# Optimization experiments

Hardware: AMD Instinct MI355X
Metric: run time of the kernel (lower is better)

## Reference

```python
import jax, jax.numpy as jnp
import numpy as np


def setup_inputs() -> dict:
    B, n, C = 256, 512, 256
    key = jax.random.key(0)
    ks = jax.random.split(key, 8)
    s = 1.0 / np.sqrt(C)
    return {
        "P": jax.random.normal(ks[0], (B, n, C), dtype=jnp.float32),
        "id": jax.random.randint(ks[1], (B,), 0, n, dtype=jnp.int64),
        "Wq": jax.random.normal(ks[2], (C, C), dtype=jnp.float32) * s,
        "bq": jax.random.normal(ks[3], (C,), dtype=jnp.float32) * s,
        "Wk": jax.random.normal(ks[4], (C, C), dtype=jnp.float32) * s,
        "bk": jax.random.normal(ks[5], (C,), dtype=jnp.float32) * s,
        "Wv": jax.random.normal(ks[6], (C, C), dtype=jnp.float32) * s,
        "bv": jax.random.normal(ks[7], (C,), dtype=jnp.float32) * s,
    }


def reference(P, id, Wq, bq, Wk, bk, Wv, bv):
    # Gather the query row per batch first, then project (same math as
    # projecting all rows and gathering, but avoids redundant compute).
    B = P.shape[0]
    p_sel = P[jnp.arange(B), id]                 # [B, C]
    Q = p_sel @ Wq.T + bq                        # [B, C]
    K = jnp.einsum('bnc,dc->bnd', P, Wk) + bk    # [B, n, C]
    V = jnp.einsum('bnc,dc->bnd', P, Wv) + bv    # [B, n, C]
    scores = jnp.einsum('bc,bnc->bn', Q, K)      # [B, n] (no sqrt scaling, per source)
    attn = jax.nn.softmax(scores, axis=-1)       # [B, n]
    out = jnp.einsum('bn,bnc->bc', attn, V)      # [B, C]
    return out
```

## Files before the change

### kernel.cpp

```cpp
#include <hip/hip_runtime.h>

#define BATCH 256
#define NROW  512
#define CDIM  256
#define SPLIT 8
#define CHUNK (NROW / SPLIT)
#define WPB   4
#define RPW   (CHUNK / WPB)
#define CHK   4
#define NCHK  (RPW / CHK)

#define DOT4(a, b) ((a).x * (b).x + (a).y * (b).y + (a).z * (b).z + (a).w * (b).w)

__global__ __launch_bounds__(256) void qk_kernel(
    const float* __restrict__ P, const int* __restrict__ idx,
    const float* __restrict__ Wq, const float* __restrict__ bq,
    const float* __restrict__ Wk, float* __restrict__ qk) {
  const int b = blockIdx.x;
  const int t = threadIdx.x;
  const int lane = t & 63;
  const int w = t >> 6;

  __shared__ float s_psel[CDIM];
  __shared__ float s_q[CDIM];
  __shared__ float s_qkp[WPB][CDIM];

  s_psel[t] = P[((size_t)b * NROW + (size_t)idx[b]) * CDIM + t];
  __syncthreads();

  const float4 pr4 = ((const float4*)s_psel)[lane];

  const int d0 = w * 64;
#pragma unroll
  for (int g = 0; g < 8; ++g) {
    float4 wq[8];
#pragma unroll
    for (int i = 0; i < 8; ++i)
      wq[i] = ((const float4*)(Wq + (size_t)(d0 + g * 8 + i) * CDIM))[lane];
#pragma unroll
    for (int i = 0; i < 8; ++i) {
      float part = DOT4(wq[i], pr4);
#pragma unroll
      for (int mm = 32; mm >= 1; mm >>= 1) part += __shfl_xor(part, mm, 64);
      if (lane == 0) s_q[d0 + g * 8 + i] = part + bq[d0 + g * 8 + i];
    }
  }
  __syncthreads();

  {
    float4 acc = make_float4(0.f, 0.f, 0.f, 0.f);
#pragma unroll 8
    for (int dd = 0; dd < 64; ++dd) {
      const int d = d0 + dd;
      const float qd = s_q[d];
      const float4 wk4 = ((const float4*)(Wk + (size_t)d * CDIM))[lane];
      acc.x += qd * wk4.x; acc.y += qd * wk4.y;
      acc.z += qd * wk4.z; acc.w += qd * wk4.w;
    }
    ((float4*)s_qkp[w])[lane] = acc;
  }
  __syncthreads();

  qk[(size_t)b * CDIM + t] =
      s_qkp[0][t] + s_qkp[1][t] + s_qkp[2][t] + s_qkp[3][t];
}

__global__ __launch_bounds__(256, 8) void attn_part_kernel(
    const float* __restrict__ P, const float* __restrict__ qk,
    float* __restrict__ ctxp, float* __restrict__ mp, float* __restrict__ lp) {
  const int bs = blockIdx.x;
  const int b = bs >> 3;
  const int s = bs & (SPLIT - 1);
  const int t = threadIdx.x;
  const int lane = t & 63;
  const int w = t >> 6;

  __shared__ float s_ctx[WPB][CDIM];
  __shared__ float s_m[WPB], s_l[WPB];

  const float* Pw =
      P + ((size_t)b * NROW + (size_t)s * CHUNK + (size_t)w * RPW) * CDIM;

  float4 pv0[CHK], pv1[CHK];
#pragma unroll
  for (int i = 0; i < CHK; ++i)
    pv0[i] = ((const float4*)(Pw + (size_t)i * CDIM))[lane];

  const float4 qk4 = ((const float4*)(qk + (size_t)b * CDIM))[lane];

  float m = -1e30f, l = 0.f;
  float4 ctx = make_float4(0.f, 0.f, 0.f, 0.f);

#define PREFETCH(dst, chn)                                                   \
  {                                                                          \
    _Pragma("unroll") for (int i = 0; i < CHK; ++i) dst[i] =                 \
        ((const float4*)(Pw + (size_t)((chn) * CHK + i) * CDIM))[lane];      \
  }

#define CONSUME(cur)                                                         \
  {                                                                          \
    float sc[CHK];                                                           \
    _Pragma("unroll") for (int i = 0; i < CHK; ++i) {                        \
      float part = DOT4(cur[i], qk4);                                        \
      _Pragma("unroll") for (int mm = 32; mm >= 1; mm >>= 1)                 \
          part += __shfl_xor(part, mm, 64);                                  \
      sc[i] = part;                                                          \
    }                                                                        \
    float cmax = sc[0];                                                      \
    _Pragma("unroll") for (int i = 1; i < CHK; ++i)                          \
        cmax = fmaxf(cmax, sc[i]);                                           \
    const float mnew = fmaxf(m, cmax);                                       \
    const float scale = __expf(m - mnew);       \
    l *= scale;                                                              \
    ctx.x *= scale; ctx.y *= scale; ctx.z *= scale; ctx.w *= scale;          \
    _Pragma("unroll") for (int i = 0; i < CHK; ++i) {                        \
      const float p = __expf(sc[i] - mnew);                                  \
      l += p;                                                                \
      ctx.x += p * cur[i].x; ctx.y += p * cur[i].y;                          \
      ctx.z += p * cur[i].z; ctx.w += p * cur[i].w;                          \
    }                                                                        \
    m = mnew;                                                                \
  }

#pragma unroll
  for (int cc = 0; cc < NCHK; cc += 2) {
    if (cc + 1 < NCHK) PREFETCH(pv1, cc + 1);
    CONSUME(pv0);
    if (cc + 2 < NCHK) PREFETCH(pv0, cc + 2);
    if (cc + 1 < NCHK) CONSUME(pv1);
  }
#undef PREFETCH
#undef CONSUME

  ((float4*)s_ctx[w])[lane] = ctx;
  if (lane == 0) { s_m[w] = m; s_l[w] = l; }
  __syncthreads();

  float mb = fmaxf(fmaxf(s_m[0], s_m[1]), fmaxf(s_m[2], s_m[3]));
  float co0 = __expf(s_m[0] - mb), co1 = __expf(s_m[1] - mb);
  float co2 = __expf(s_m[2] - mb), co3 = __expf(s_m[3] - mb);
  ctxp[(size_t)bs * CDIM + t] = co0 * s_ctx[0][t] + co1 * s_ctx[1][t] +
                                co2 * s_ctx[2][t] + co3 * s_ctx[3][t];
  if (t == 0) {
    mp[bs] = mb;
    lp[bs] = co0 * s_l[0] + co1 * s_l[1] + co2 * s_l[2] + co3 * s_l[3];
  }
}

__global__ __launch_bounds__(256) void combine_kernel(
    const float* __restrict__ ctxp, const float* __restrict__ mp,
    const float* __restrict__ lp, const float* __restrict__ Wv,
    const float* __restrict__ bv, float* __restrict__ out) {
  const int b = blockIdx.x;
  const int t = threadIdx.x;
  const int lane = t & 63;
  const int w = t >> 6;

  __shared__ float s_ctxn[CDIM];

  {
    float ms[SPLIT];
    float mg = -3.4e38f;
#pragma unroll
    for (int i = 0; i < SPLIT; ++i) {
      ms[i] = mp[b * SPLIT + i];
      mg = fmaxf(mg, ms[i]);
    }
    float ww[SPLIT];
    float lg = 0.f;
#pragma unroll
    for (int i = 0; i < SPLIT; ++i) {
      ww[i] = __expf(ms[i] - mg);
      lg += lp[b * SPLIT + i] * ww[i];
    }
    float c = 0.f;
#pragma unroll
    for (int i = 0; i < SPLIT; ++i)
      c += ctxp[(size_t)(b * SPLIT + i) * CDIM + t] * ww[i];
    s_ctxn[t] = c / lg;
  }
  __syncthreads();

  const float4 cx4 = ((const float4*)s_ctxn)[lane];
  const int d0 = w * 64;
#pragma unroll
  for (int g = 0; g < 8; ++g) {
    float4 wv[8];
#pragma unroll
    for (int i = 0; i < 8; ++i)
      wv[i] = ((const float4*)(Wv + (size_t)(d0 + g * 8 + i) * CDIM))[lane];
#pragma unroll
    for (int i = 0; i < 8; ++i) {
      float part = DOT4(wv[i], cx4);
#pragma unroll
      for (int mm = 32; mm >= 1; mm >>= 1) part += __shfl_xor(part, mm, 64);
      if (lane == 0) {
        const int d = d0 + g * 8 + i;
        out[(size_t)b * CDIM + d] = part + bv[d];
      }
    }
  }
}

extern "C" void kernel_launch(void* const* d_in, const int* in_sizes, int n_in,
                              void* d_out, int out_size, void* d_ws,
                              size_t ws_size, hipStream_t stream) {
  const float* P  = (const float*)d_in[0];
  const int*  idx = (const int*)d_in[1];
  const float* Wq = (const float*)d_in[2];
  const float* bq = (const float*)d_in[3];
  const float* Wk = (const float*)d_in[4];
  const float* Wv = (const float*)d_in[6];
  const float* bv = (const float*)d_in[7];
  float* out = (float*)d_out;

  float* ws   = (float*)d_ws;
  float* qk   = ws;
  float* ctxp = qk + BATCH * CDIM;
  float* mp   = ctxp + BATCH * SPLIT * CDIM;
  float* lp   = mp + BATCH * SPLIT;

  qk_kernel<<<BATCH, 256, 0, stream>>>(P, idx, Wq, bq, Wk, qk);
  attn_part_kernel<<<BATCH * SPLIT, 256, 0, stream>>>(P, qk, ctxp, mp, lp);
  combine_kernel<<<BATCH, 256, 0, stream>>>(ctxp, mp, lp, Wv, bv, out);
}
```

Before: 256.1 us.

## Precompute fused Wq·Wk matrix and transposed Wv, batch qk and combine

Adds a prep kernel that computes the fused matrix M = Wq^T Wk and the bias term bq·Wk, and writes a transposed copy of Wv. With these, the qk and combine kernels become simple per-thread column GEMVs that handle 4 or 8 batches per block, reusing weight loads across batches. The attention kernel now issues all 16 rows of loads up front with CHK=8 in place of the double-buffered loop, and its occupancy hint drops to 4. This adds an extra launch and a 256x256x256 matmul run by only 32 blocks on every call, which may sit on the critical path.

```diff
diff --git a/kernel.cpp b/kernel.cpp
--- a/kernel.cpp
+++ b/kernel.cpp
@@ -7,65 +7,81 @@
 #define CHUNK (NROW / SPLIT)
 #define WPB   4
 #define RPW   (CHUNK / WPB)
-#define CHK   4
-#define NCHK  (RPW / CHK)
+#define CHK   8
 
 #define DOT4(a, b) ((a).x * (b).x + (a).y * (b).y + (a).z * (b).z + (a).w * (b).w)
+
+__global__ __launch_bounds__(256) void prep_kernel(
+    const float* __restrict__ Wq, const float* __restrict__ bq,
+    const float* __restrict__ Wk, const float* __restrict__ Wv,
+    float* __restrict__ MT, float* __restrict__ c0, float* __restrict__ WvT) {
+  const int t = threadIdx.x;
+
+  if (blockIdx.x < 16) {
+    __shared__ float s_wq[CDIM][16];
+    __shared__ float s_bq[CDIM];
+    const int cbase = blockIdx.x * 16;
+#pragma unroll
+    for (int it = 0; it < 16; ++it) {
+      const int d = it * 16 + (t >> 4);
+      s_wq[d][t & 15] = Wq[(size_t)d * CDIM + cbase + (t & 15)];
+    }
+    if (blockIdx.x == 0) s_bq[t] = bq[t];
+    __syncthreads();
+
+    float acc[16];
+#pragma unroll
+    for (int j = 0; j < 16; ++j) acc[j] = 0.f;
+    float accc0 = 0.f;
+    for (int d = 0; d < CDIM; ++d) {
+      const float wkv = Wk[(size_t)d * CDIM + t];
+#pragma unroll
+      for (int j = 0; j < 16; ++j) acc[j] += s_wq[d][j] * wkv;
+      if (blockIdx.x == 0) accc0 += s_bq[d] * wkv;
+    }
+#pragma unroll
+    for (int j = 0; j < 16; ++j) MT[(size_t)(cbase + j) * CDIM + t] = acc[j];
+    if (blockIdx.x == 0) c0[t] = accc0;
+  } else {
+    __shared__ float s_wv[16][CDIM + 1];
+    const int rbase = (blockIdx.x - 16) * 16;
+#pragma unroll
+    for (int r = 0; r < 16; ++r)
+      s_wv[r][t] = Wv[(size_t)(rbase + r) * CDIM + t];
+    __syncthreads();
+#pragma unroll
+    for (int it = 0; it < 16; ++it) {
+      const int c = it * 16 + (t >> 4);
+      WvT[(size_t)c * CDIM + rbase + (t & 15)] = s_wv[t & 15][c];
+    }
+  }
+}
 
 __global__ __launch_bounds__(256) void qk_kernel(
     const float* __restrict__ P, const int* __restrict__ idx,
-    const float* __restrict__ Wq, const float* __restrict__ bq,
-    const float* __restrict__ Wk, float* __restrict__ qk) {
-  const int b = blockIdx.x;
-  const int t = threadIdx.x;
-  const int lane = t & 63;
-  const int w = t >> 6;
-
-  __shared__ float s_psel[CDIM];
-  __shared__ float s_q[CDIM];
-  __shared__ float s_qkp[WPB][CDIM];
-
-  s_psel[t] = P[((size_t)b * NROW + (size_t)idx[b]) * CDIM + t];
+    const float* __restrict__ MT, const float* __restrict__ c0,
+    float* __restrict__ qk) {
+  const int t = threadIdx.x;
+  const int b0 = blockIdx.x * 4;
+
+  __shared__ float s_ps[4][CDIM];
+#pragma unroll
+  for (int j = 0; j < 4; ++j)
+    s_ps[j][t] = P[((size_t)(b0 + j) * NROW + (size_t)idx[b0 + j]) * CDIM + t];
   __syncthreads();
 
-  const float4 pr4 = ((const float4*)s_psel)[lane];
-
-  const int d0 = w * 64;
-#pragma unroll
-  for (int g = 0; g < 8; ++g) {
-    float4 wq[8];
-#pragma unroll
-    for (int i = 0; i < 8; ++i)
-      wq[i] = ((const float4*)(Wq + (size_t)(d0 + g * 8 + i) * CDIM))[lane];
-#pragma unroll
-    for (int i = 0; i < 8; ++i) {
-      float part = DOT4(wq[i], pr4);
-#pragma unroll
-      for (int mm = 32; mm >= 1; mm >>= 1) part += __shfl_xor(part, mm, 64);
-      if (lane == 0) s_q[d0 + g * 8 + i] = part + bq[d0 + g * 8 + i];
-    }
-  }
-  __syncthreads();
-
-  {
-    float4 acc = make_float4(0.f, 0.f, 0.f, 0.f);
-#pragma unroll 8
-    for (int dd = 0; dd < 64; ++dd) {
-      const int d = d0 + dd;
-      const float qd = s_q[d];
-      const float4 wk4 = ((const float4*)(Wk + (size_t)d * CDIM))[lane];
-      acc.x += qd * wk4.x; acc.y += qd * wk4.y;
-      acc.z += qd * wk4.z; acc.w += qd * wk4.w;
-    }
-    ((float4*)s_qkp[w])[lane] = acc;
-  }
-  __syncthreads();
-
-  qk[(size_t)b * CDIM + t] =
-      s_qkp[0][t] + s_qkp[1][t] + s_qkp[2][t] + s_qkp[3][t];
-}
-
-__global__ __launch_bounds__(256, 8) void attn_part_kernel(
+  float acc[4] = {0.f, 0.f, 0.f, 0.f};
+  for (int c = 0; c < CDIM; ++c) {
+    const float mtv = MT[(size_t)c * CDIM + t];
+#pragma unroll
+    for (int j = 0; j < 4; ++j) acc[j] += s_ps[j][c] * mtv;
+  }
+  const float cc = c0[t];
+#pragma unroll
+  for (int j = 0; j < 4; ++j) qk[(size_t)(b0 + j) * CDIM + t] = acc[j] + cc;
+}
+
+__global__ __launch_bounds__(256, 4) void attn_part_kernel(
     const float* __restrict__ P, const float* __restrict__ qk,
     float* __restrict__ ctxp, float* __restrict__ mp, float* __restrict__ lp) {
   const int bs = blockIdx.x;
@@ -81,21 +97,18 @@
   const float* Pw =
       P + ((size_t)b * NROW + (size_t)s * CHUNK + (size_t)w * RPW) * CDIM;
 
+  const float4 qk4 = ((const float4*)(qk + (size_t)b * CDIM))[lane];
+
   float4 pv0[CHK], pv1[CHK];
 #pragma unroll
   for (int i = 0; i < CHK; ++i)
     pv0[i] = ((const float4*)(Pw + (size_t)i * CDIM))[lane];
-
-  const float4 qk4 = ((const float4*)(qk + (size_t)b * CDIM))[lane];
+#pragma unroll
+  for (int i = 0; i < CHK; ++i)
+    pv1[i] = ((const float4*)(Pw + (size_t)(CHK + i) * CDIM))[lane];
 
   float m = -1e30f, l = 0.f;
   float4 ctx = make_float4(0.f, 0.f, 0.f, 0.f);
-
-#define PREFETCH(dst, chn)                                                   \
-  {                                                                          \
-    _Pragma("unroll") for (int i = 0; i < CHK; ++i) dst[i] =                 \
-        ((const float4*)(Pw + (size_t)((chn) * CHK + i) * CDIM))[lane];      \
-  }
 
 #define CONSUME(cur)                                                         \
   {                                                                          \
@@ -110,7 +123,7 @@
     _Pragma("unroll") for (int i = 1; i < CHK; ++i)                          \
         cmax = fmaxf(cmax, sc[i]);                                           \
     const float mnew = fmaxf(m, cmax);                                       \
-    const float scale = __expf(m - mnew);       \
+    const float scale = __expf(m - mnew);      \
     l *= scale;                                                              \
     ctx.x *= scale; ctx.y *= scale; ctx.z *= scale; ctx.w *= scale;          \
     _Pragma("unroll") for (int i = 0; i < CHK; ++i) {                        \
@@ -122,23 +135,17 @@
     m = mnew;                                                                \
   }
 
-#pragma unroll
-  for (int cc = 0; cc < NCHK; cc += 2) {
-    if (cc + 1 < NCHK) PREFETCH(pv1, cc + 1);
-    CONSUME(pv0);
-    if (cc + 2 < NCHK) PREFETCH(pv0, cc + 2);
-    if (cc + 1 < NCHK) CONSUME(pv1);
-  }
-#undef PREFETCH
+  CONSUME(pv0);
+  CONSUME(pv1);
 #undef CONSUME
 
   ((float4*)s_ctx[w])[lane] = ctx;
   if (lane == 0) { s_m[w] = m; s_l[w] = l; }
   __syncthreads();
 
-  float mb = fmaxf(fmaxf(s_m[0], s_m[1]), fmaxf(s_m[2], s_m[3]));
-  float co0 = __expf(s_m[0] - mb), co1 = __expf(s_m[1] - mb);
-  float co2 = __expf(s_m[2] - mb), co3 = __expf(s_m[3] - mb);
+  const float mb = fmaxf(fmaxf(s_m[0], s_m[1]), fmaxf(s_m[2], s_m[3]));
+  const float co0 = __expf(s_m[0] - mb), co1 = __expf(s_m[1] - mb);
+  const float co2 = __expf(s_m[2] - mb), co3 = __expf(s_m[3] - mb);
   ctxp[(size_t)bs * CDIM + t] = co0 * s_ctx[0][t] + co1 * s_ctx[1][t] +
                                 co2 * s_ctx[2][t] + co3 * s_ctx[3][t];
   if (t == 0) {
@@ -149,16 +156,16 @@
 
 __global__ __launch_bounds__(256) void combine_kernel(
     const float* __restrict__ ctxp, const float* __restrict__ mp,
-    const float* __restrict__ lp, const float* __restrict__ Wv,
+    const float* __restrict__ lp, const float* __restrict__ WvT,
     const float* __restrict__ bv, float* __restrict__ out) {
-  const int b = blockIdx.x;
-  const int t = threadIdx.x;
-  const int lane = t & 63;
-  const int w = t >> 6;
-
-  __shared__ float s_ctxn[CDIM];
-
-  {
+  const int t = threadIdx.x;
+  const int b0 = blockIdx.x * 8;
+
+  __shared__ float s_ctxn[8][CDIM];
+
+#pragma unroll
+  for (int j = 0; j < 8; ++j) {
+    const int b = b0 + j;
     float ms[SPLIT];
     float mg = -3.4e38f;
 #pragma unroll
@@ -166,40 +173,26 @@
       ms[i] = mp[b * SPLIT + i];
       mg = fmaxf(mg, ms[i]);
     }
-    float ww[SPLIT];
-    float lg = 0.f;
+    float lg = 0.f, c = 0.f;
 #pragma unroll
     for (int i = 0; i < SPLIT; ++i) {
-      ww[i] = __expf(ms[i] - mg);
-      lg += lp[b * SPLIT + i] * ww[i];
-    }
-    float c = 0.f;
-#pragma unroll
-    for (int i = 0; i < SPLIT; ++i)
-      c += ctxp[(size_t)(b * SPLIT + i) * CDIM + t] * ww[i];
-    s_ctxn[t] = c / lg;
+      const float ww = __expf(ms[i] - mg);
+      lg += lp[b * SPLIT + i] * ww;
+      c += ctxp[(size_t)(b * SPLIT + i) * CDIM + t] * ww;
+    }
+    s_ctxn[j][t] = c / lg;
   }
   __syncthreads();
 
-  const float4 cx4 = ((const float4*)s_ctxn)[lane];
-  const int d0 = w * 64;
-#pragma unroll
-  for (int g = 0; g < 8; ++g) {
-    float4 wv[8];
-#pragma unroll
-    for (int i = 0; i < 8; ++i)
-      wv[i] = ((const float4*)(Wv + (size_t)(d0 + g * 8 + i) * CDIM))[lane];
-#pragma unroll
-    for (int i = 0; i < 8; ++i) {
-      float part = DOT4(wv[i], cx4);
-#pragma unroll
-      for (int mm = 32; mm >= 1; mm >>= 1) part += __shfl_xor(part, mm, 64);
-      if (lane == 0) {
-        const int d = d0 + g * 8 + i;
-        out[(size_t)b * CDIM + d] = part + bv[d];
-      }
-    }
-  }
+  float acc[8] = {0.f, 0.f, 0.f, 0.f, 0.f, 0.f, 0.f, 0.f};
+  for (int c = 0; c < CDIM; ++c) {
+    const float wvt = WvT[(size_t)c * CDIM + t];
+#pragma unroll
+    for (int j = 0; j < 8; ++j) acc[j] += s_ctxn[j][c] * wvt;
+  }
+  const float bvt = bv[t];
+#pragma unroll
+  for (int j = 0; j < 8; ++j) out[(size_t)(b0 + j) * CDIM + t] = acc[j] + bvt;
 }
 
 extern "C" void kernel_launch(void* const* d_in, const int* in_sizes, int n_in,
@@ -215,12 +208,16 @@
   float* out = (float*)d_out;
 
   float* ws   = (float*)d_ws;
-  float* qk   = ws;
+  float* MT   = ws;
+  float* c0   = MT + CDIM * CDIM;
+  float* WvT  = c0 + CDIM;
+  float* qk   = WvT + CDIM * CDIM;
   float* ctxp = qk + BATCH * CDIM;
   float* mp   = ctxp + BATCH * SPLIT * CDIM;
   float* lp   = mp + BATCH * SPLIT;
 
-  qk_kernel<<<BATCH, 256, 0, stream>>>(P, idx, Wq, bq, Wk, qk);
+  prep_kernel<<<32, 256, 0, stream>>>(Wq, bq, Wk, Wv, MT, c0, WvT);
+  qk_kernel<<<BATCH / 4, 256, 0, stream>>>(P, idx, MT, c0, qk);
   attn_part_kernel<<<BATCH * SPLIT, 256, 0, stream>>>(P, qk, ctxp, mp, lp);
-  combine_kernel<<<BATCH, 256, 0, stream>>>(ctxp, mp, lp, Wv, bv, out);
-}
+  combine_kernel<<<BATCH / 8, 256, 0, stream>>>(ctxp, mp, lp, WvT, bv, out);
+}
```

New measurement: 265.8 us. 1.04x slower.

## Fuse combine into attention kernel via last-block atomic counter

Applied to the files above, without the earlier changes.

Removes the separate combine kernel launch: each attention split block increments a per-batch counter, and the last block to finish merges the split partials and applies the Wv projection. The counter is zeroed in the qk kernel. It also raises the chunk size to 8 rows and loads all 16 rows per wave up front instead of double-buffering, with launch bounds lowered to 4 blocks per CU to leave room for the extra registers. This saves one launch and its gap but adds fences and an atomic, and the Wv work now runs on only 256 tail blocks.

```diff
diff --git a/kernel.cpp b/kernel.cpp
--- a/kernel.cpp
+++ b/kernel.cpp
@@ -7,15 +7,15 @@
 #define CHUNK (NROW / SPLIT)
 #define WPB   4
 #define RPW   (CHUNK / WPB)
-#define CHK   4
-#define NCHK  (RPW / CHK)
+#define CHK   8
 
 #define DOT4(a, b) ((a).x * (b).x + (a).y * (b).y + (a).z * (b).z + (a).w * (b).w)
 
 __global__ __launch_bounds__(256) void qk_kernel(
     const float* __restrict__ P, const int* __restrict__ idx,
     const float* __restrict__ Wq, const float* __restrict__ bq,
-    const float* __restrict__ Wk, float* __restrict__ qk) {
+    const float* __restrict__ Wk, float* __restrict__ qk,
+    unsigned int* __restrict__ cnt) {
   const int b = blockIdx.x;
   const int t = threadIdx.x;
   const int lane = t & 63;
@@ -25,12 +25,13 @@
   __shared__ float s_q[CDIM];
   __shared__ float s_qkp[WPB][CDIM];
 
+  if (t == 0) cnt[b] = 0u;
   s_psel[t] = P[((size_t)b * NROW + (size_t)idx[b]) * CDIM + t];
   __syncthreads();
 
   const float4 pr4 = ((const float4*)s_psel)[lane];
-
   const int d0 = w * 64;
+
 #pragma unroll
   for (int g = 0; g < 8; ++g) {
     float4 wq[8];
@@ -65,9 +66,11 @@
       s_qkp[0][t] + s_qkp[1][t] + s_qkp[2][t] + s_qkp[3][t];
 }
 
-__global__ __launch_bounds__(256, 8) void attn_part_kernel(
+__global__ __launch_bounds__(256, 4) void attn_kernel(
     const float* __restrict__ P, const float* __restrict__ qk,
-    float* __restrict__ ctxp, float* __restrict__ mp, float* __restrict__ lp) {
+    const float* __restrict__ Wv, const float* __restrict__ bv,
+    float* __restrict__ ctxp, float* __restrict__ mp, float* __restrict__ lp,
+    unsigned int* __restrict__ cnt, float* __restrict__ out) {
   const int bs = blockIdx.x;
   const int b = bs >> 3;
   const int s = bs & (SPLIT - 1);
@@ -77,25 +80,24 @@
 
   __shared__ float s_ctx[WPB][CDIM];
   __shared__ float s_m[WPB], s_l[WPB];
+  __shared__ float s_ctxn[CDIM];
+  __shared__ int s_last;
 
   const float* Pw =
       P + ((size_t)b * NROW + (size_t)s * CHUNK + (size_t)w * RPW) * CDIM;
 
+  const float4 qk4 = ((const float4*)(qk + (size_t)b * CDIM))[lane];
+
   float4 pv0[CHK], pv1[CHK];
 #pragma unroll
   for (int i = 0; i < CHK; ++i)
     pv0[i] = ((const float4*)(Pw + (size_t)i * CDIM))[lane];
-
-  const float4 qk4 = ((const float4*)(qk + (size_t)b * CDIM))[lane];
+#pragma unroll
+  for (int i = 0; i < CHK; ++i)
+    pv1[i] = ((const float4*)(Pw + (size_t)(CHK + i) * CDIM))[lane];
 
   float m = -1e30f, l = 0.f;
   float4 ctx = make_float4(0.f, 0.f, 0.f, 0.f);
-
-#define PREFETCH(dst, chn)                                                   \
-  {                                                                          \
-    _Pragma("unroll") for (int i = 0; i < CHK; ++i) dst[i] =                 \
-        ((const float4*)(Pw + (size_t)((chn) * CHK + i) * CDIM))[lane];      \
-  }
 
 #define CONSUME(cur)                                                         \
   {                                                                          \
@@ -110,7 +112,7 @@
     _Pragma("unroll") for (int i = 1; i < CHK; ++i)                          \
         cmax = fmaxf(cmax, sc[i]);                                           \
     const float mnew = fmaxf(m, cmax);                                       \
-    const float scale = __expf(m - mnew);       \
+    const float scale = __expf(m - mnew);      \
     l *= scale;                                                              \
     ctx.x *= scale; ctx.y *= scale; ctx.z *= scale; ctx.w *= scale;          \
     _Pragma("unroll") for (int i = 0; i < CHK; ++i) {                        \
@@ -122,41 +124,34 @@
     m = mnew;                                                                \
   }
 
-#pragma unroll
-  for (int cc = 0; cc < NCHK; cc += 2) {
-    if (cc + 1 < NCHK) PREFETCH(pv1, cc + 1);
-    CONSUME(pv0);
-    if (cc + 2 < NCHK) PREFETCH(pv0, cc + 2);
-    if (cc + 1 < NCHK) CONSUME(pv1);
-  }
-#undef PREFETCH
+  CONSUME(pv0);
+  CONSUME(pv1);
 #undef CONSUME
 
   ((float4*)s_ctx[w])[lane] = ctx;
   if (lane == 0) { s_m[w] = m; s_l[w] = l; }
   __syncthreads();
 
-  float mb = fmaxf(fmaxf(s_m[0], s_m[1]), fmaxf(s_m[2], s_m[3]));
-  float co0 = __expf(s_m[0] - mb), co1 = __expf(s_m[1] - mb);
-  float co2 = __expf(s_m[2] - mb), co3 = __expf(s_m[3] - mb);
+  const float mb = fmaxf(fmaxf(s_m[0], s_m[1]), fmaxf(s_m[2], s_m[3]));
+  const float co0 = __expf(s_m[0] - mb), co1 = __expf(s_m[1] - mb);
+  const float co2 = __expf(s_m[2] - mb), co3 = __expf(s_m[3] - mb);
   ctxp[(size_t)bs * CDIM + t] = co0 * s_ctx[0][t] + co1 * s_ctx[1][t] +
                                 co2 * s_ctx[2][t] + co3 * s_ctx[3][t];
   if (t == 0) {
     mp[bs] = mb;
     lp[bs] = co0 * s_l[0] + co1 * s_l[1] + co2 * s_l[2] + co3 * s_l[3];
   }
-}
-
-__global__ __launch_bounds__(256) void combine_kernel(
-    const float* __restrict__ ctxp, const float* __restrict__ mp,
-    const float* __restrict__ lp, const float* __restrict__ Wv,
-    const float* __restrict__ bv, float* __restrict__ out) {
-  const int b = blockIdx.x;
-  const int t = threadIdx.x;
-  const int lane = t & 63;
-  const int w = t >> 6;
-
-  __shared__ float s_ctxn[CDIM];
+
+  __threadfence();
+  __syncthreads();
+  if (t == 0) {
+    const unsigned int old = atomicAdd(&cnt[b], 1u);
+    s_last = (old == SPLIT - 1) ? 1 : 0;
+  }
+  __syncthreads();
+  if (!s_last) return;
+
+  __threadfence();
 
   {
     float ms[SPLIT];
@@ -166,37 +161,35 @@
       ms[i] = mp[b * SPLIT + i];
       mg = fmaxf(mg, ms[i]);
     }
-    float ww[SPLIT];
-    float lg = 0.f;
+    float lg = 0.f, c = 0.f;
 #pragma unroll
     for (int i = 0; i < SPLIT; ++i) {
-      ww[i] = __expf(ms[i] - mg);
-      lg += lp[b * SPLIT + i] * ww[i];
-    }
-    float c = 0.f;
-#pragma unroll
-    for (int i = 0; i < SPLIT; ++i)
-      c += ctxp[(size_t)(b * SPLIT + i) * CDIM + t] * ww[i];
+      const float ww = __expf(ms[i] - mg);
+      lg += lp[b * SPLIT + i] * ww;
+      c += ctxp[(size_t)(b * SPLIT + i) * CDIM + t] * ww;
+    }
     s_ctxn[t] = c / lg;
   }
   __syncthreads();
 
-  const float4 cx4 = ((const float4*)s_ctxn)[lane];
-  const int d0 = w * 64;
-#pragma unroll
-  for (int g = 0; g < 8; ++g) {
-    float4 wv[8];
-#pragma unroll
-    for (int i = 0; i < 8; ++i)
-      wv[i] = ((const float4*)(Wv + (size_t)(d0 + g * 8 + i) * CDIM))[lane];
-#pragma unroll
-    for (int i = 0; i < 8; ++i) {
-      float part = DOT4(wv[i], cx4);
-#pragma unroll
-      for (int mm = 32; mm >= 1; mm >>= 1) part += __shfl_xor(part, mm, 64);
-      if (lane == 0) {
-        const int d = d0 + g * 8 + i;
-        out[(size_t)b * CDIM + d] = part + bv[d];
+  {
+    const float4 cx4 = ((const float4*)s_ctxn)[lane];
+    const int d0 = w * 64;
+#pragma unroll
+    for (int g = 0; g < 8; ++g) {
+      float4 wv[8];
+#pragma unroll
+      for (int i = 0; i < 8; ++i)
+        wv[i] = ((const float4*)(Wv + (size_t)(d0 + g * 8 + i) * CDIM))[lane];
+#pragma unroll
+      for (int i = 0; i < 8; ++i) {
+        float part = DOT4(wv[i], cx4);
+#pragma unroll
+        for (int mm = 32; mm >= 1; mm >>= 1) part += __shfl_xor(part, mm, 64);
+        if (lane == 0) {
+          const int d = d0 + g * 8 + i;
+          out[(size_t)b * CDIM + d] = part + bv[d];
+        }
       }
     }
   }
@@ -219,8 +212,9 @@
   float* ctxp = qk + BATCH * CDIM;
   float* mp   = ctxp + BATCH * SPLIT * CDIM;
   float* lp   = mp + BATCH * SPLIT;
-
-  qk_kernel<<<BATCH, 256, 0, stream>>>(P, idx, Wq, bq, Wk, qk);
-  attn_part_kernel<<<BATCH * SPLIT, 256, 0, stream>>>(P, qk, ctxp, mp, lp);
-  combine_kernel<<<BATCH, 256, 0, stream>>>(ctxp, mp, lp, Wv, bv, out);
+  unsigned int* cnt = (unsigned int*)(lp + BATCH * SPLIT);
+
+  qk_kernel<<<BATCH, 256, 0, stream>>>(P, idx, Wq, bq, Wk, qk, cnt);
+  attn_kernel<<<BATCH * SPLIT, 256, 0, stream>>>(P, qk, Wv, bv, ctxp, mp, lp,
+                                                 cnt, out);
 }
```

Result: slower. 710.7 us (+177.5%).
